# Kernel tuning notes

Measured on AMD Instinct MI355X. Metric: run time of the kernel, lower is better.

Reference implementation:

```python
import jax, jax.numpy as jnp
import numpy as np

B, D, T = 8, 1024, 512
HID, NH, NL = 256, 4, 2
OUT = HID // NH  # 64 per-head dim
ALPHA = 0.2      # leaky relu slope
EPS = 1e-5       # layernorm eps


def setup_inputs() -> dict:
    key = jax.random.key(0)
    ks = jax.random.split(key, 10)
    X_obs = jax.random.normal(ks[0], (B, D, T), dtype=jnp.float32)
    mask = (jax.random.uniform(ks[1], (B, D, T)) < 0.8).astype(jnp.float32)
    W_in = jax.random.normal(ks[2], (2 * T, HID), dtype=jnp.float32) * (1.0 / np.sqrt(2 * T))
    b_in = jnp.zeros((HID,), dtype=jnp.float32)
    gat_W = jax.random.normal(ks[3], (NL, NH, HID, OUT), dtype=jnp.float32) * (1.0 / np.sqrt(HID))
    gat_a = jax.random.normal(ks[4], (NL, NH, 2 * OUT), dtype=jnp.float32) * 0.1
    ln_g = jnp.ones((NL, HID), dtype=jnp.float32)
    ln_b = jnp.zeros((NL, HID), dtype=jnp.float32)
    W_out = jax.random.normal(ks[5], (HID, T), dtype=jnp.float32) * (1.0 / np.sqrt(HID))
    b_out = jnp.zeros((T,), dtype=jnp.float32)
    return dict(X_obs=X_obs, mask=mask, W_in=W_in, b_in=b_in, gat_W=gat_W,
                gat_a=gat_a, ln_g=ln_g, ln_b=ln_b, W_out=W_out, b_out=b_out)


def _layer_norm(x, g, b):
    mu = jnp.mean(x, axis=-1, keepdims=True)
    var = jnp.mean((x - mu) ** 2, axis=-1, keepdims=True)
    return (x - mu) * jax.lax.rsqrt(var + EPS) * g + b


def _gat_forward(X_obs, mask, W_in, b_in, gat_W, gat_a, ln_g, ln_b, W_out, b_out):
    # mean-impute per (d, t) position across batch
    obs_sum = jnp.sum(X_obs * mask, axis=0, keepdims=True)
    obs_cnt = jnp.sum(mask, axis=0, keepdims=True)
    pos_mean = obs_sum / (obs_cnt + 1e-10)
    X_mean = X_obs * mask + (1.0 - mask) * pos_mean

    x = jnp.concatenate([X_mean, mask], axis=-1)       # (B, D, 2T)
    h = x @ W_in + b_in                                 # (B, N, HID)

    for l in range(NL):
        Wl = gat_W[l]                                   # (H, HID, OUT)
        a_left = gat_a[l, :, :OUT]                      # (H, OUT)
        a_right = gat_a[l, :, OUT:]                     # (H, OUT)
        hW = jnp.einsum('bnd,hde->bhne', h, Wl)         # (B, H, N, OUT)
        # e_ij = leakyrelu(a_left . h_i + a_right . h_j) -- avoids O(N^2 * 2d) concat
        s_l = jnp.einsum('bhne,he->bhn', hW, a_left)
        s_r = jnp.einsum('bhne,he->bhn', hW, a_right)
        e = jax.nn.leaky_relu(s_l[..., :, None] + s_r[..., None, :], ALPHA)  # (B,H,N,N)
        attn = jax.nn.softmax(e, axis=-1)
        head_out = jnp.einsum('bhnm,bhme->bhne', attn, hW)                   # (B,H,N,OUT)
        h_new = jnp.transpose(head_out, (0, 2, 1, 3)).reshape(h.shape[0], h.shape[1], HID)
        h = _layer_norm(h + h_new, ln_g[l], ln_b[l])

    return h @ W_out + b_out                            # (B, D, T)


def reference(X_obs, mask, W_in, b_in, gat_W, gat_a, ln_g, ln_b, W_out, b_out):
    return _gat_forward(X_obs, mask, W_in, b_in, gat_W, gat_a, ln_g, ln_b, W_out, b_out)
```

## Files before the change

kernel.cpp:

```cpp
#include <hip/hip_runtime.h>
#include <hip/hip_bf16.h>

constexpr int B_   = 8;
constexpr int D_   = 1024;
constexpr int T_   = 512;
constexpr int HID_ = 256;
constexpr int NH_  = 4;
constexpr int NL_  = 2;
constexpr float ALPHA_ = 0.2f;
constexpr float EPS_   = 1e-5f;
constexpr int OUT_ = 64;
constexpr int M_ = B_ * D_;
constexpr int DT_ = D_ * T_;
constexpr int KIN_ = 2 * T_;

typedef __attribute__((ext_vector_type(8))) short short8;
typedef __attribute__((ext_vector_type(4))) float floatx4;

__device__ __forceinline__ unsigned short f2bf(float f) {
    unsigned int u = __float_as_uint(f);
    unsigned int r = u + 0x7fffu + ((u >> 16) & 1u);
    return (unsigned short)(r >> 16);
}
__device__ __forceinline__ unsigned int kenc(float f) {
    unsigned int u = __float_as_uint(f);
    return (u & 0x80000000u) ? ~u : (u | 0x80000000u);
}
__device__ __forceinline__ float kdec(unsigned int k) {
    unsigned int u = (k & 0x80000000u) ? (k ^ 0x80000000u) : ~k;
    return __uint_as_float(u);
}

__global__ __launch_bounds__(256) void prep_k(const float* __restrict__ X,
                                              const float* __restrict__ Mk,
                                              const float* __restrict__ W_in,
                                              const float* __restrict__ gatW,
                                              const float* __restrict__ W_out,
                                              unsigned short* __restrict__ Ain,
                                              unsigned short* __restrict__ Wt_in,
                                              unsigned short* __restrict__ Wcat,
                                              unsigned short* __restrict__ WtO,
                                              unsigned int* __restrict__ rmaxkey) {
    int bx = blockIdx.x;
    if (bx < 512) {
        int idx4 = (bx * 256 + threadIdx.x) * 4;
        int t = idx4 & (T_ - 1);
        int d = idx4 >> 9;
        float4 x[B_], m[B_];
        float4 s = {0, 0, 0, 0}, c = {0, 0, 0, 0};
#pragma unroll
        for (int b = 0; b < B_; b++) {
            x[b] = *(const float4*)&X[(size_t)b * DT_ + idx4];
            m[b] = *(const float4*)&Mk[(size_t)b * DT_ + idx4];
            s.x += x[b].x * m[b].x; s.y += x[b].y * m[b].y;
            s.z += x[b].z * m[b].z; s.w += x[b].w * m[b].w;
            c.x += m[b].x; c.y += m[b].y; c.z += m[b].z; c.w += m[b].w;
        }
        float4 pm;
        pm.x = s.x / (c.x + 1e-10f); pm.y = s.y / (c.y + 1e-10f);
        pm.z = s.z / (c.z + 1e-10f); pm.w = s.w / (c.w + 1e-10f);
#pragma unroll
        for (int b = 0; b < B_; b++) {
            size_t row = (size_t)b * D_ + d;
            ushort4 xm, mk;
            xm.x = f2bf(x[b].x * m[b].x + (1.f - m[b].x) * pm.x);
            xm.y = f2bf(x[b].y * m[b].y + (1.f - m[b].y) * pm.y);
            xm.z = f2bf(x[b].z * m[b].z + (1.f - m[b].z) * pm.z);
            xm.w = f2bf(x[b].w * m[b].w + (1.f - m[b].w) * pm.w);
            mk.x = f2bf(m[b].x); mk.y = f2bf(m[b].y);
            mk.z = f2bf(m[b].z); mk.w = f2bf(m[b].w);
            *(ushort4*)&Ain[row * KIN_ + t]      = xm;
            *(ushort4*)&Ain[row * KIN_ + T_ + t] = mk;
        }
    } else {
        int idx = (bx - 512) * 256 + threadIdx.x;
        if (idx < 64) rmaxkey[idx] = 0u;
        if (idx < 262144) {
            int n = idx >> 10, k = idx & 1023;
            Wt_in[idx] = f2bf(W_in[(size_t)k * HID_ + n]);
        } else if (idx < 393216) {
            int j = idx - 262144;
            int l = j >> 16, n = (j >> 8) & 255, k = j & 255;
            int h = n >> 6, e = n & 63;
            Wcat[j] = f2bf(gatW[(((size_t)(l * NH_ + h) * HID_) + k) * OUT_ + e]);
        } else {
            int j = idx - 393216;
            int n = j >> 8, k = j & 255;
            WtO[j] = f2bf(W_out[(size_t)k * T_ + n]);
        }
    }
}

template <int MODE>
__global__ __launch_bounds__(256) void gemm_bf16_k(
        const unsigned short* __restrict__ A,
        const unsigned short* __restrict__ Bt,
        const float* __restrict__ bias,
        float* __restrict__ C,
        unsigned short* __restrict__ Cb,
        const float* __restrict__ ga,
        float* __restrict__ s_l,
        float* __restrict__ s_r,
        unsigned int* __restrict__ rmaxkey,
        int Nsz, int Ksz) {
    __shared__ __align__(16) unsigned short As[2][64 * 72];
    __shared__ __align__(16) unsigned short Bs[2][64 * 72];
    int tid = threadIdx.x;
    int wave = tid >> 6, lane = tid & 63;
    int q = lane >> 4, r16 = lane & 15;
    int rowbase = blockIdx.y * 64;
    int colbase = blockIdx.x * 64;

    int srow = tid >> 3, sk = (tid & 7) * 8;
    const unsigned short* Ap0 = A + (size_t)(rowbase + srow) * Ksz + sk;
    const unsigned short* Ap1 = A + (size_t)(rowbase + srow + 32) * Ksz + sk;
    const unsigned short* Bp0 = Bt + (size_t)(colbase + srow) * Ksz + sk;
    const unsigned short* Bp1 = Bt + (size_t)(colbase + srow + 32) * Ksz + sk;
    int la0 = srow * 72 + sk, la1 = (srow + 32) * 72 + sk;

    floatx4 acc[4];
#pragma unroll
    for (int i = 0; i < 4; i++) acc[i] = (floatx4)0.f;

    uint4 pa0 = *(const uint4*)Ap0, pa1 = *(const uint4*)Ap1;
    uint4 pb0 = *(const uint4*)Bp0, pb1 = *(const uint4*)Bp1;
    *(uint4*)&As[0][la0] = pa0;
    *(uint4*)&As[0][la1] = pa1;
    *(uint4*)&Bs[0][la0] = pb0;
    *(uint4*)&Bs[0][la1] = pb1;

    int nk = Ksz >> 6;
    for (int it = 0; it < nk; it++) {
        int cur = it & 1;
        __syncthreads();
        if (it + 1 < nk) {
            int kt = (it + 1) << 6;
            pa0 = *(const uint4*)(Ap0 + kt);
            pa1 = *(const uint4*)(Ap1 + kt);
            pb0 = *(const uint4*)(Bp0 + kt);
            pb1 = *(const uint4*)(Bp1 + kt);
        }
#pragma unroll
        for (int t = 0; t < 2; t++) {
            short8 a = *(const short8*)&As[cur][(wave * 16 + r16) * 72 + t * 32 + q * 8];
#pragma unroll
            for (int ni = 0; ni < 4; ni++) {
                short8 b = *(const short8*)&Bs[cur][(ni * 16 + r16) * 72 + t * 32 + q * 8];
                acc[ni] = __builtin_amdgcn_mfma_f32_16x16x32_bf16(a, b, acc[ni], 0, 0, 0);
            }
        }
        if (it + 1 < nk) {
            int nxt = cur ^ 1;
            *(uint4*)&As[nxt][la0] = pa0;
            *(uint4*)&As[nxt][la1] = pa1;
            *(uint4*)&Bs[nxt][la0] = pb0;
            *(uint4*)&Bs[nxt][la1] = pb1;
        }
    }
    if constexpr (MODE == 2) {
        int bhh = ((rowbase >> 10) << 2) + blockIdx.x;
        int nb = (rowbase & (D_ - 1)) + wave * 16;
#pragma unroll
        for (int ni = 0; ni < 4; ni++) {
            int e = ni * 16 + r16;
            ushort4 pk;
            pk.x = f2bf(acc[ni][0]);
            pk.y = f2bf(acc[ni][1]);
            pk.z = f2bf(acc[ni][2]);
            pk.w = f2bf(acc[ni][3]);
            *(ushort4*)&Cb[((size_t)(bhh * 64 + e) << 10) + nb + q * 4] = pk;
        }
        const float* gab = ga + blockIdx.x * 2 * OUT_;
        float al4[4], ar4[4];
#pragma unroll
        for (int ni = 0; ni < 4; ni++) {
            al4[ni] = gab[ni * 16 + r16];
            ar4[ni] = gab[OUT_ + ni * 16 + r16];
        }
        float slv[4], srv[4];
#pragma unroll
        for (int rr = 0; rr < 4; rr++) {
            float s1 = 0.f, s2 = 0.f;
#pragma unroll
            for (int ni = 0; ni < 4; ni++) {
                s1 += acc[ni][rr] * al4[ni];
                s2 += acc[ni][rr] * ar4[ni];
            }
            slv[rr] = s1;
            srv[rr] = s2;
        }
#pragma unroll
        for (int off = 1; off < 16; off <<= 1) {
#pragma unroll
            for (int rr = 0; rr < 4; rr++) {
                slv[rr] += __shfl_xor(slv[rr], off, 64);
                srv[rr] += __shfl_xor(srv[rr], off, 64);
            }
        }
        {
            int rsel = r16 & 3;
            float sv = (rsel == 0) ? slv[0] : (rsel == 1) ? slv[1] : (rsel == 2) ? slv[2] : slv[3];
            float rv = (rsel == 0) ? srv[0] : (rsel == 1) ? srv[1] : (rsel == 2) ? srv[2] : srv[3];
            int n = nb + q * 4 + rsel;
            if (r16 < 4)                 s_l[bhh * D_ + n] = sv;
            else if (r16 >= 8 && r16 < 12) s_r[bhh * D_ + n] = rv;
        }
        float mx = fmaxf(fmaxf(srv[0], srv[1]), fmaxf(srv[2], srv[3]));
        mx = fmaxf(mx, __shfl_xor(mx, 16, 64));
        mx = fmaxf(mx, __shfl_xor(mx, 32, 64));
        if (lane == 0) atomicMax(&rmaxkey[bhh], kenc(mx));
    } else {
#pragma unroll
        for (int rr = 0; rr < 4; rr++) {
            int row = rowbase + wave * 16 + q * 4 + rr;
#pragma unroll
            for (int ni = 0; ni < 4; ni++) {
                int col = colbase + ni * 16 + r16;
                float v = acc[ni][rr] + (bias ? bias[col] : 0.f);
                C[(size_t)row * Nsz + col] = v;
                if constexpr (MODE == 1) Cb[(size_t)row * Nsz + col] = f2bf(v);
            }
        }
    }
}

__global__ __launch_bounds__(256) void attn_k(const unsigned short* __restrict__ hwT,
                                              const float* __restrict__ sl_g,
                                              const float* __restrict__ sr_g,
                                              const unsigned int* __restrict__ rmaxkey,
                                              float* __restrict__ pacc,
                                              float* __restrict__ pden) {
    int bh = blockIdx.x;
    int b = bh >> 2, h = bh & 3;
    int half = blockIdx.z;
    int mb = half * 512;
    int tid = threadIdx.x;
    int wave = tid >> 6, lane = tid & 63;
    int q = lane >> 4, r16 = lane & 15;

    __shared__ float srs[512];
    __shared__ __align__(16) unsigned short Vt[2][64][136];

    *(float2*)&srs[tid * 2] = *(const float2*)&sr_g[bh * D_ + mb + tid * 2];

    float rm = kdec(rmaxkey[bh]);
    int row0 = blockIdx.y * 64 + wave * 16;
    float sl = sl_g[bh * D_ + row0 + r16];
    float xm = sl + rm;
    float Mn = fmaxf(xm, ALPHA_ * xm);

    floatx4 acc[4];
#pragma unroll
    for (int i = 0; i < 4; i++) acc[i] = (floatx4)0.f;
    float dsum = 0.f;

    const unsigned short* vbase = hwT + ((size_t)(bh * 64) << 10) + mb;
    int se[4], sp[4];
#pragma unroll
    for (int i = 0; i < 4; i++) {
        int s = tid + i * 256;
        se[i] = s >> 4;
        sp[i] = (s & 15) * 8;
    }

    uint4 pre[4];
#pragma unroll
    for (int i = 0; i < 4; i++)
        pre[i] = *(const uint4*)&vbase[((size_t)se[i] << 10) + sp[i]];
#pragma unroll
    for (int i = 0; i < 4; i++)
        *(uint4*)&Vt[0][se[i]][sp[i]] = pre[i];
    __syncthreads();

    for (int c = 0; c < 4; c++) {
        int cur = c & 1;
        if (c < 3) {
            int mo = (c + 1) * 128;
#pragma unroll
            for (int i = 0; i < 4; i++)
                pre[i] = *(const uint4*)&vbase[((size_t)se[i] << 10) + mo + sp[i]];
        }
#pragma unroll
        for (int kk = 0; kk < 128; kk += 32) {
            int m0 = c * 128 + kk + q * 8;
            float4 s0 = *(const float4*)&srs[m0];
            float4 s1 = *(const float4*)&srs[m0 + 4];
            float sr8[8] = {s0.x, s0.y, s0.z, s0.w, s1.x, s1.y, s1.z, s1.w};
            float p[8];
#pragma unroll
            for (int j = 0; j < 8; j++) {
                float x = sl + sr8[j];
                float e = fmaxf(x, ALPHA_ * x);
                float pj = __expf(e - Mn);
                dsum += pj;
                p[j] = pj;
            }
            union { unsigned int u[4]; short8 s8; } cv;
#pragma unroll
            for (int j = 0; j < 4; j++) {
                unsigned int lo = (__float_as_uint(p[2 * j]) + 0x8000u) >> 16;
                unsigned int hi = (__float_as_uint(p[2 * j + 1]) + 0x8000u) & 0xffff0000u;
                cv.u[j] = hi | lo;
            }
#pragma unroll
            for (int ni = 0; ni < 4; ni++) {
                short8 bfr = *(const short8*)&Vt[cur][ni * 16 + r16][kk + q * 8];
                acc[ni] = __builtin_amdgcn_mfma_f32_16x16x32_bf16(cv.s8, bfr, acc[ni], 0, 0, 0);
            }
        }
        if (c < 3) {
#pragma unroll
            for (int i = 0; i < 4; i++)
                *(uint4*)&Vt[cur ^ 1][se[i]][sp[i]] = pre[i];
        }
        __syncthreads();
    }
    dsum += __shfl_xor(dsum, 16);
    dsum += __shfl_xor(dsum, 32);
    size_t gr0 = (size_t)b * D_ + row0;
    if (lane < 16) pden[((size_t)half * M_ + gr0 + r16) * NH_ + h] = dsum;
#pragma unroll
    for (int rr = 0; rr < 4; rr++) {
        size_t grow = gr0 + q * 4 + rr;
#pragma unroll
        for (int ni = 0; ni < 4; ni++) {
            pacc[((size_t)half * M_ + grow) * HID_ + h * OUT_ + ni * 16 + r16] = acc[ni][rr];
        }
    }
}

__global__ __launch_bounds__(256) void addln_k(float* __restrict__ h,
                                               const float* __restrict__ pacc,
                                               const float* __restrict__ pden,
                                               const float* __restrict__ g,
                                               const float* __restrict__ bb,
                                               unsigned short* __restrict__ hbf) {
    int wave = threadIdx.x >> 6, lane = threadIdx.x & 63;
    size_t row = (size_t)blockIdx.x * 4 + wave;
    float4 a  = *(const float4*)&h[row * HID_ + lane * 4];
    float4 p0 = *(const float4*)&pacc[row * HID_ + lane * 4];
    float4 p1 = *(const float4*)&pacc[((size_t)M_ + row) * HID_ + lane * 4];
    int hh = lane >> 4;
    float den = pden[row * NH_ + hh] + pden[((size_t)M_ + row) * NH_ + hh];
    float inv = 1.f / den;
    float4 v = {a.x + (p0.x + p1.x) * inv, a.y + (p0.y + p1.y) * inv,
                a.z + (p0.z + p1.z) * inv, a.w + (p0.w + p1.w) * inv};
    float s = v.x + v.y + v.z + v.w;
#pragma unroll
    for (int off = 1; off < 64; off <<= 1) s += __shfl_xor(s, off, 64);
    float mu = s * (1.f / HID_);
    float4 d = {v.x - mu, v.y - mu, v.z - mu, v.w - mu};
    float s2 = d.x * d.x + d.y * d.y + d.z * d.z + d.w * d.w;
#pragma unroll
    for (int off = 1; off < 64; off <<= 1) s2 += __shfl_xor(s2, off, 64);
    float rs = rsqrtf(s2 * (1.f / HID_) + EPS_);
    float4 gg = *(const float4*)&g[lane * 4];
    float4 bbv = *(const float4*)&bb[lane * 4];
    float4 res;
    res.x = d.x * rs * gg.x + bbv.x;
    res.y = d.y * rs * gg.y + bbv.y;
    res.z = d.z * rs * gg.z + bbv.z;
    res.w = d.w * rs * gg.w + bbv.w;
    *(float4*)&h[row * HID_ + lane * 4] = res;
    ushort4 pk = {f2bf(res.x), f2bf(res.y), f2bf(res.z), f2bf(res.w)};
    *(ushort4*)&hbf[row * HID_ + lane * 4] = pk;
}

extern "C" void kernel_launch(void* const* d_in, const int* in_sizes, int n_in,
                              void* d_out, int out_size, void* d_ws, size_t ws_size,
                              hipStream_t stream) {
    const float* X_obs = (const float*)d_in[0];
    const float* mask  = (const float*)d_in[1];
    const float* W_in  = (const float*)d_in[2];
    const float* b_in  = (const float*)d_in[3];
    const float* gat_W = (const float*)d_in[4];
    const float* gat_a = (const float*)d_in[5];
    const float* ln_g  = (const float*)d_in[6];
    const float* ln_b  = (const float*)d_in[7];
    const float* W_out = (const float*)d_in[8];
    const float* b_out = (const float*)d_in[9];
    float* out = (float*)d_out;

    char* base = (char*)d_ws;
    unsigned short* Ain  = (unsigned short*)base;
    unsigned short* hwT  = (unsigned short*)base;
    float* pacc = (float*)(base + (4u << 20));
    float* pden = (float*)(base + (20u << 20));
    float* hbuf = (float*)(base + (21u << 20));
    unsigned short* hbf   = (unsigned short*)(base + (29u << 20));
    unsigned short* Wt_in = (unsigned short*)(base + (33u << 20));
    unsigned short* Wcat  = Wt_in + (size_t)HID_ * KIN_;
    unsigned short* WtO   = Wcat + (size_t)NL_ * HID_ * HID_;
    float* slb = (float*)(WtO + (size_t)T_ * HID_);
    float* srb = slb + B_ * NH_ * D_;
    unsigned int* rmaxkey = (unsigned int*)(srb + B_ * NH_ * D_);

    prep_k<<<2560, 256, 0, stream>>>(X_obs, mask, W_in, gat_W, W_out,
                                     Ain, Wt_in, Wcat, WtO, rmaxkey);

    gemm_bf16_k<1><<<dim3(HID_ / 64, M_ / 64), 256, 0, stream>>>(
        Ain, Wt_in, b_in, hbuf, hbf, nullptr, nullptr, nullptr, nullptr,
        HID_, KIN_);

    for (int l = 0; l < NL_; l++) {
        gemm_bf16_k<2><<<dim3(HID_ / 64, M_ / 64), 256, 0, stream>>>(
            hbf, Wcat + (size_t)l * HID_ * HID_, nullptr, nullptr, hwT,
            gat_a + (size_t)l * NH_ * 2 * OUT_, slb, srb, rmaxkey + l * 32,
            HID_, HID_);
        attn_k<<<dim3(B_ * NH_, D_ / 64, 2), 256, 0, stream>>>(
            hwT, slb, srb, rmaxkey + l * 32, pacc, pden);
        addln_k<<<M_ / 4, 256, 0, stream>>>(hbuf, pacc, pden,
                                            ln_g + (size_t)l * HID_,
                                            ln_b + (size_t)l * HID_, hbf);
    }

    gemm_bf16_k<0><<<dim3(T_ / 64, M_ / 64), 256, 0, stream>>>(
        hbf, WtO, b_out, out, nullptr, nullptr, nullptr, nullptr, nullptr,
        T_, HID_);
}
```

Before: 217.0 us.

## Replace dense GAT attention with sorted prefix-sum decomposition of leaky-relu softmax

Uses the rank-1 structure of the attention logits (s_l[i] + s_r[j] through a piecewise-linear leaky relu). Each (batch, head) sorts s_r and builds prefix sums of exp-weighted values for both slopes. Each row then binary-searches its breakpoint and combines the two prefix sums, turning O(N^2) attention into O(N log N). This removes the dense MFMA attention kernel and fuses the residual add and layernorm into the row kernel. In exchange it adds a single-block-per-head bitonic sort and serial prefix scans with low parallelism, and it changes numerical behaviour by subtracting large prefix sums.

```diff
diff --git a/kernel.cpp b/kernel.cpp
--- a/kernel.cpp
+++ b/kernel.cpp
@@ -13,6 +13,7 @@
 constexpr int M_ = B_ * D_;
 constexpr int DT_ = D_ * T_;
 constexpr int KIN_ = 2 * T_;
+constexpr int CKS_ = 132;
 
 typedef __attribute__((ext_vector_type(8))) short short8;
 typedef __attribute__((ext_vector_type(4))) float floatx4;
@@ -21,6 +22,9 @@
     unsigned int u = __float_as_uint(f);
     unsigned int r = u + 0x7fffu + ((u >> 16) & 1u);
     return (unsigned short)(r >> 16);
+}
+__device__ __forceinline__ float bf2f(unsigned short u) {
+    return __uint_as_float(((unsigned int)u) << 16);
 }
 __device__ __forceinline__ unsigned int kenc(float f) {
     unsigned int u = __float_as_uint(f);
@@ -163,12 +167,11 @@
 #pragma unroll
         for (int ni = 0; ni < 4; ni++) {
             int e = ni * 16 + r16;
-            ushort4 pk;
-            pk.x = f2bf(acc[ni][0]);
-            pk.y = f2bf(acc[ni][1]);
-            pk.z = f2bf(acc[ni][2]);
-            pk.w = f2bf(acc[ni][3]);
-            *(ushort4*)&Cb[((size_t)(bhh * 64 + e) << 10) + nb + q * 4] = pk;
+#pragma unroll
+            for (int rr = 0; rr < 4; rr++) {
+                int m = nb + q * 4 + rr;
+                Cb[((size_t)bhh << 16) + ((size_t)m << 6) + e] = f2bf(acc[ni][rr]);
+            }
         }
         const float* gab = ga + blockIdx.x * 2 * OUT_;
         float al4[4], ar4[4];
@@ -224,146 +227,183 @@
     }
 }
 
-__global__ __launch_bounds__(256) void attn_k(const unsigned short* __restrict__ hwT,
-                                              const float* __restrict__ sl_g,
-                                              const float* __restrict__ sr_g,
-                                              const unsigned int* __restrict__ rmaxkey,
-                                              float* __restrict__ pacc,
-                                              float* __restrict__ pden) {
-    int bh = blockIdx.x;
-    int b = bh >> 2, h = bh & 3;
-    int half = blockIdx.z;
-    int mb = half * 512;
+__global__ __launch_bounds__(512) void sortprefix_k(
+        const unsigned short* __restrict__ hwN,
+        const float* __restrict__ sr_g,
+        const unsigned int* __restrict__ rmaxkey,
+        float* __restrict__ srt,
+        int* __restrict__ sig,
+        float* __restrict__ wm,
+        float* __restrict__ ck) {
+    __shared__ float skey[1024];
+    __shared__ int   sidx[1024];
+    __shared__ float w1s[1024], w2s[1024];
+    __shared__ float csum[8][64][2];
+    __shared__ float csca[8][2];
+    int bh = blockIdx.x, tid = threadIdx.x;
+    for (int t = tid; t < 1024; t += 512) { skey[t] = sr_g[bh * D_ + t]; sidx[t] = t; }
+    __syncthreads();
+    for (int k = 2; k <= 1024; k <<= 1) {
+        for (int j = k >> 1; j > 0; j >>= 1) {
+            for (int t = tid; t < 1024; t += 512) {
+                int ixj = t ^ j;
+                if (ixj > t) {
+                    bool up = ((t & k) == 0);
+                    float a = skey[t], b = skey[ixj];
+                    bool sw = up ? (a > b) : (a < b);
+                    if (sw) {
+                        skey[t] = b; skey[ixj] = a;
+                        int ti = sidx[t]; sidx[t] = sidx[ixj]; sidx[ixj] = ti;
+                    }
+                }
+            }
+            __syncthreads();
+        }
+    }
+    float rm = kdec(rmaxkey[bh]);
+    for (int t = tid; t < 1024; t += 512) {
+        float u = skey[t] - rm;
+        float w1 = __expf(u), w2 = __expf(ALPHA_ * u);
+        w1s[t] = w1; w2s[t] = w2;
+        srt[bh * D_ + t] = skey[t];
+        sig[bh * D_ + t] = sidx[t];
+        *(float2*)&wm[(size_t)(bh * D_ + t) * 2] = float2{w1, w2};
+    }
+    __syncthreads();
+    int e = tid & 63, c = tid >> 6;
+    const unsigned short* vb = hwN + ((size_t)bh << 16);
+    int t0 = c * 128;
+    float a1 = 0.f, a2 = 0.f, q1 = 0.f, q2 = 0.f;
+    for (int t = t0; t < t0 + 128; ++t) {
+        float v = bf2f(vb[((size_t)sidx[t] << 6) + e]);
+        a1 = fmaf(w1s[t], v, a1);
+        a2 = fmaf(w2s[t], v, a2);
+    }
+    csum[c][e][0] = a1; csum[c][e][1] = a2;
+    if (e == 0) {
+        for (int t = t0; t < t0 + 128; ++t) { q1 += w1s[t]; q2 += w2s[t]; }
+        csca[c][0] = q1; csca[c][1] = q2;
+    }
+    __syncthreads();
+    float r1 = 0.f, r2 = 0.f, p1 = 0.f, p2 = 0.f;
+    for (int cc = 0; cc < c; ++cc) { r1 += csum[cc][e][0]; r2 += csum[cc][e][1]; }
+    if (e == 0) {
+        for (int cc = 0; cc < c; ++cc) { p1 += csca[cc][0]; p2 += csca[cc][1]; }
+    }
+    float* ckb = ck + (size_t)bh * 257 * CKS_;
+    for (int t = t0; t < t0 + 128; ++t) {
+        if ((t & 3) == 0) {
+            *(float2*)&ckb[(size_t)(t >> 2) * CKS_ + 2 * e] = float2{r1, r2};
+            if (e == 0) *(float2*)&ckb[(size_t)(t >> 2) * CKS_ + 128] = float2{p1, p2};
+        }
+        float v = bf2f(vb[((size_t)sidx[t] << 6) + e]);
+        r1 = fmaf(w1s[t], v, r1);
+        r2 = fmaf(w2s[t], v, r2);
+        if (e == 0) { p1 += w1s[t]; p2 += w2s[t]; }
+    }
+    if (c == 7) {
+        *(float2*)&ckb[(size_t)256 * CKS_ + 2 * e] = float2{r1, r2};
+        if (e == 0) *(float2*)&ckb[(size_t)256 * CKS_ + 128] = float2{p1, p2};
+    }
+}
+
+__global__ __launch_bounds__(128) void rowln_k(
+        float* __restrict__ h,
+        const float* __restrict__ sl_g,
+        const unsigned int* __restrict__ rmaxkey,
+        const float* __restrict__ srt,
+        const int* __restrict__ sig,
+        const float* __restrict__ wm,
+        const float* __restrict__ ck,
+        const unsigned short* __restrict__ hwN,
+        const float* __restrict__ g,
+        const float* __restrict__ bb,
+        unsigned short* __restrict__ hbf) {
+    __shared__ float srtL[4][1024];
+    __shared__ float hnew[32][260];
+    int blk = blockIdx.x;
+    int b = blk >> 5;
+    int d0 = (blk & 31) << 5;
     int tid = threadIdx.x;
-    int wave = tid >> 6, lane = tid & 63;
-    int q = lane >> 4, r16 = lane & 15;
-
-    __shared__ float srs[512];
-    __shared__ __align__(16) unsigned short Vt[2][64][136];
-
-    *(float2*)&srs[tid * 2] = *(const float2*)&sr_g[bh * D_ + mb + tid * 2];
-
+    for (int i = tid; i < 4096; i += 128)
+        srtL[i >> 10][i & 1023] = srt[(size_t)((b * 4 + (i >> 10)) * D_) + (i & 1023)];
+    __syncthreads();
+    int r = tid & 31, h4 = tid >> 5;
+    int bh = b * 4 + h4;
+    int d = d0 + r;
+    float sl = sl_g[bh * D_ + d];
     float rm = kdec(rmaxkey[bh]);
-    int row0 = blockIdx.y * 64 + wave * 16;
-    float sl = sl_g[bh * D_ + row0 + r16];
-    float xm = sl + rm;
-    float Mn = fmaxf(xm, ALPHA_ * xm);
-
-    floatx4 acc[4];
-#pragma unroll
-    for (int i = 0; i < 4; i++) acc[i] = (floatx4)0.f;
-    float dsum = 0.f;
-
-    const unsigned short* vbase = hwT + ((size_t)(bh * 64) << 10) + mb;
-    int se[4], sp[4];
-#pragma unroll
-    for (int i = 0; i < 4; i++) {
-        int s = tid + i * 256;
-        se[i] = s >> 4;
-        sp[i] = (s & 15) * 8;
-    }
-
-    uint4 pre[4];
-#pragma unroll
-    for (int i = 0; i < 4; i++)
-        pre[i] = *(const uint4*)&vbase[((size_t)se[i] << 10) + sp[i]];
-#pragma unroll
-    for (int i = 0; i < 4; i++)
-        *(uint4*)&Vt[0][se[i]][sp[i]] = pre[i];
+    float x = sl + rm;
+    float Mn = fmaxf(x, ALPHA_ * x);
+    float A  = __expf(x - Mn);
+    float B2 = __expf(ALPHA_ * x - Mn);
+    float key = -sl;
+    int lo = 0, hi = 1024;
+    while (lo < hi) {
+        int mid = (lo + hi) >> 1;
+        if (srtL[h4][mid] < key) lo = mid + 1; else hi = mid;
+    }
+    int t = lo;
+    int c4 = t >> 2, nf = t & 3;
+    const float* ckb = ck + ((size_t)bh * 257 + c4) * CKS_;
+    const float* ckT = ck + ((size_t)bh * 257 + 256) * CKS_;
+    float2 qs = *(const float2*)&ckb[128];
+    float2 qT = *(const float2*)&ckT[128];
+    float w1f[3], w2f[3];
+    const unsigned short* vp[3];
+#pragma unroll
+    for (int f = 0; f < 3; ++f) {
+        w1f[f] = 0.f; w2f[f] = 0.f; vp[f] = hwN;
+        if (f < nf) {
+            int rk = c4 * 4 + f;
+            float2 ww = *(const float2*)&wm[(size_t)(bh * D_ + rk) * 2];
+            w1f[f] = ww.x; w2f[f] = ww.y;
+            vp[f] = hwN + ((size_t)bh << 16) + ((size_t)sig[bh * D_ + rk] << 6);
+            qs.x += ww.x; qs.y += ww.y;
+        }
+    }
+    float den = A * (qT.x - qs.x) + B2 * qs.y;
+    float inv = 1.f / den;
+    for (int e = 0; e < 64; ++e) {
+        float2 p  = *(const float2*)&ckb[2 * e];
+        float2 Tt = *(const float2*)&ckT[2 * e];
+#pragma unroll
+        for (int f = 0; f < 3; ++f) {
+            if (f < nf) {
+                float v = bf2f(vp[f][e]);
+                p.x = fmaf(w1f[f], v, p.x);
+                p.y = fmaf(w2f[f], v, p.y);
+            }
+        }
+        hnew[r][h4 * 64 + e] = (A * (Tt.x - p.x) + B2 * p.y) * inv;
+    }
     __syncthreads();
-
-    for (int c = 0; c < 4; c++) {
-        int cur = c & 1;
-        if (c < 3) {
-            int mo = (c + 1) * 128;
-#pragma unroll
-            for (int i = 0; i < 4; i++)
-                pre[i] = *(const uint4*)&vbase[((size_t)se[i] << 10) + mo + sp[i]];
-        }
-#pragma unroll
-        for (int kk = 0; kk < 128; kk += 32) {
-            int m0 = c * 128 + kk + q * 8;
-            float4 s0 = *(const float4*)&srs[m0];
-            float4 s1 = *(const float4*)&srs[m0 + 4];
-            float sr8[8] = {s0.x, s0.y, s0.z, s0.w, s1.x, s1.y, s1.z, s1.w};
-            float p[8];
-#pragma unroll
-            for (int j = 0; j < 8; j++) {
-                float x = sl + sr8[j];
-                float e = fmaxf(x, ALPHA_ * x);
-                float pj = __expf(e - Mn);
-                dsum += pj;
-                p[j] = pj;
-            }
-            union { unsigned int u[4]; short8 s8; } cv;
-#pragma unroll
-            for (int j = 0; j < 4; j++) {
-                unsigned int lo = (__float_as_uint(p[2 * j]) + 0x8000u) >> 16;
-                unsigned int hi = (__float_as_uint(p[2 * j + 1]) + 0x8000u) & 0xffff0000u;
-                cv.u[j] = hi | lo;
-            }
-#pragma unroll
-            for (int ni = 0; ni < 4; ni++) {
-                short8 bfr = *(const short8*)&Vt[cur][ni * 16 + r16][kk + q * 8];
-                acc[ni] = __builtin_amdgcn_mfma_f32_16x16x32_bf16(cv.s8, bfr, acc[ni], 0, 0, 0);
-            }
-        }
-        if (c < 3) {
-#pragma unroll
-            for (int i = 0; i < 4; i++)
-                *(uint4*)&Vt[cur ^ 1][se[i]][sp[i]] = pre[i];
-        }
-        __syncthreads();
-    }
-    dsum += __shfl_xor(dsum, 16);
-    dsum += __shfl_xor(dsum, 32);
-    size_t gr0 = (size_t)b * D_ + row0;
-    if (lane < 16) pden[((size_t)half * M_ + gr0 + r16) * NH_ + h] = dsum;
-#pragma unroll
-    for (int rr = 0; rr < 4; rr++) {
-        size_t grow = gr0 + q * 4 + rr;
-#pragma unroll
-        for (int ni = 0; ni < 4; ni++) {
-            pacc[((size_t)half * M_ + grow) * HID_ + h * OUT_ + ni * 16 + r16] = acc[ni][rr];
-        }
-    }
-}
-
-__global__ __launch_bounds__(256) void addln_k(float* __restrict__ h,
-                                               const float* __restrict__ pacc,
-                                               const float* __restrict__ pden,
-                                               const float* __restrict__ g,
-                                               const float* __restrict__ bb,
-                                               unsigned short* __restrict__ hbf) {
-    int wave = threadIdx.x >> 6, lane = threadIdx.x & 63;
-    size_t row = (size_t)blockIdx.x * 4 + wave;
-    float4 a  = *(const float4*)&h[row * HID_ + lane * 4];
-    float4 p0 = *(const float4*)&pacc[row * HID_ + lane * 4];
-    float4 p1 = *(const float4*)&pacc[((size_t)M_ + row) * HID_ + lane * 4];
-    int hh = lane >> 4;
-    float den = pden[row * NH_ + hh] + pden[((size_t)M_ + row) * NH_ + hh];
-    float inv = 1.f / den;
-    float4 v = {a.x + (p0.x + p1.x) * inv, a.y + (p0.y + p1.y) * inv,
-                a.z + (p0.z + p1.z) * inv, a.w + (p0.w + p1.w) * inv};
-    float s = v.x + v.y + v.z + v.w;
-#pragma unroll
-    for (int off = 1; off < 64; off <<= 1) s += __shfl_xor(s, off, 64);
-    float mu = s * (1.f / HID_);
-    float4 d = {v.x - mu, v.y - mu, v.z - mu, v.w - mu};
-    float s2 = d.x * d.x + d.y * d.y + d.z * d.z + d.w * d.w;
-#pragma unroll
-    for (int off = 1; off < 64; off <<= 1) s2 += __shfl_xor(s2, off, 64);
-    float rs = rsqrtf(s2 * (1.f / HID_) + EPS_);
-    float4 gg = *(const float4*)&g[lane * 4];
-    float4 bbv = *(const float4*)&bb[lane * 4];
-    float4 res;
-    res.x = d.x * rs * gg.x + bbv.x;
-    res.y = d.y * rs * gg.y + bbv.y;
-    res.z = d.z * rs * gg.z + bbv.z;
-    res.w = d.w * rs * gg.w + bbv.w;
-    *(float4*)&h[row * HID_ + lane * 4] = res;
-    ushort4 pk = {f2bf(res.x), f2bf(res.y), f2bf(res.z), f2bf(res.w)};
-    *(ushort4*)&hbf[row * HID_ + lane * 4] = pk;
+    int wv = tid >> 6, ln = tid & 63;
+    for (int rr = wv * 16; rr < wv * 16 + 16; ++rr) {
+        size_t grow = ((((size_t)b << 10) + d0 + rr) << 8);
+        float4 a  = *(const float4*)&h[grow + ln * 4];
+        float4 nv = *(const float4*)&hnew[rr][ln * 4];
+        float4 v = {a.x + nv.x, a.y + nv.y, a.z + nv.z, a.w + nv.w};
+        float s = v.x + v.y + v.z + v.w;
+#pragma unroll
+        for (int off = 1; off < 64; off <<= 1) s += __shfl_xor(s, off, 64);
+        float mu = s * (1.f / HID_);
+        float4 dd = {v.x - mu, v.y - mu, v.z - mu, v.w - mu};
+        float s2 = dd.x * dd.x + dd.y * dd.y + dd.z * dd.z + dd.w * dd.w;
+#pragma unroll
+        for (int off = 1; off < 64; off <<= 1) s2 += __shfl_xor(s2, off, 64);
+        float rs = rsqrtf(s2 * (1.f / HID_) + EPS_);
+        float4 gg = *(const float4*)&g[ln * 4];
+        float4 bv = *(const float4*)&bb[ln * 4];
+        float4 res;
+        res.x = dd.x * rs * gg.x + bv.x;
+        res.y = dd.y * rs * gg.y + bv.y;
+        res.z = dd.z * rs * gg.z + bv.z;
+        res.w = dd.w * rs * gg.w + bv.w;
+        *(float4*)&h[grow + ln * 4] = res;
+        ushort4 pk = {f2bf(res.x), f2bf(res.y), f2bf(res.z), f2bf(res.w)};
+        *(ushort4*)&hbf[grow + ln * 4] = pk;
+    }
 }
 
 extern "C" void kernel_launch(void* const* d_in, const int* in_sizes, int n_in,
@@ -382,10 +422,12 @@
     float* out = (float*)d_out;
 
     char* base = (char*)d_ws;
-    unsigned short* Ain  = (unsigned short*)base;
-    unsigned short* hwT  = (unsigned short*)base;
-    float* pacc = (float*)(base + (4u << 20));
-    float* pden = (float*)(base + (20u << 20));
+    unsigned short* Ain = (unsigned short*)base;
+    unsigned short* hwN = (unsigned short*)base;
+    float* ck   = (float*)(base + (5u << 20));
+    float* wm   = (float*)(base + (10u << 20));
+    float* srtb = (float*)(base + (11u << 20));
+    int*   sig  = (int*)(base + (12u << 20));
     float* hbuf = (float*)(base + (21u << 20));
     unsigned short* hbf   = (unsigned short*)(base + (29u << 20));
     unsigned short* Wt_in = (unsigned short*)(base + (33u << 20));
@@ -404,14 +446,15 @@
 
     for (int l = 0; l < NL_; l++) {
         gemm_bf16_k<2><<<dim3(HID_ / 64, M_ / 64), 256, 0, stream>>>(
-            hbf, Wcat + (size_t)l * HID_ * HID_, nullptr, nullptr, hwT,
+            hbf, Wcat + (size_t)l * HID_ * HID_, nullptr, nullptr, hwN,
             gat_a + (size_t)l * NH_ * 2 * OUT_, slb, srb, rmaxkey + l * 32,
             HID_, HID_);
-        attn_k<<<dim3(B_ * NH_, D_ / 64, 2), 256, 0, stream>>>(
-            hwT, slb, srb, rmaxkey + l * 32, pacc, pden);
-        addln_k<<<M_ / 4, 256, 0, stream>>>(hbuf, pacc, pden,
-                                            ln_g + (size_t)l * HID_,
-                                            ln_b + (size_t)l * HID_, hbf);
+        sortprefix_k<<<32, 512, 0, stream>>>(hwN, srb, rmaxkey + l * 32,
+                                             srtb, sig, wm, ck);
+        rowln_k<<<256, 128, 0, stream>>>(hbuf, slb, rmaxkey + l * 32,
+                                         srtb, sig, wm, ck, hwN,
+                                         ln_g + (size_t)l * HID_,
+                                         ln_b + (size_t)l * HID_, hbf);
     }
 
     gemm_bf16_k<0><<<dim3(T_ / 64, M_ / 64), 256, 0, stream>>>(
```

Measured after the change: 366.2 us. 1.69x slower.

## Replace dense GAT attention with sorted prefix-sum factorization of leaky-relu softmax

Applied to the files above, without the earlier changes.

Replaces the O(N^2) attention matmul with an exact factorization. Because leaky_relu(s_l+s_r) is piecewise linear, exp splits into exp(s_r) or exp(alpha*s_r) terms depending on the sign of s_l+s_r. The s_r values are bitonic-sorted per (batch, head), prefix sums of weighted V rows are built, and each row binary-searches its split point to combine two partial sums. The hW output is also transposed to node-major layout through shared memory to suit the gather. This trades tensor-core work for a serial scan in only 32 blocks of 1024 threads, which risks low occupancy and possible exp overflow or precision issues from the unnormalized weights.

```diff
diff --git a/kernel.cpp b/kernel.cpp
--- a/kernel.cpp
+++ b/kernel.cpp
@@ -21,6 +21,9 @@
     unsigned int u = __float_as_uint(f);
     unsigned int r = u + 0x7fffu + ((u >> 16) & 1u);
     return (unsigned short)(r >> 16);
+}
+__device__ __forceinline__ float bf2f(unsigned short u) {
+    return __uint_as_float(((unsigned int)u) << 16);
 }
 __device__ __forceinline__ unsigned int kenc(float f) {
     unsigned int u = __float_as_uint(f);
@@ -159,17 +162,8 @@
     }
     if constexpr (MODE == 2) {
         int bhh = ((rowbase >> 10) << 2) + blockIdx.x;
-        int nb = (rowbase & (D_ - 1)) + wave * 16;
-#pragma unroll
-        for (int ni = 0; ni < 4; ni++) {
-            int e = ni * 16 + r16;
-            ushort4 pk;
-            pk.x = f2bf(acc[ni][0]);
-            pk.y = f2bf(acc[ni][1]);
-            pk.z = f2bf(acc[ni][2]);
-            pk.w = f2bf(acc[ni][3]);
-            *(ushort4*)&Cb[((size_t)(bhh * 64 + e) << 10) + nb + q * 4] = pk;
-        }
+        int nb0 = rowbase & (D_ - 1);
+        int nb = nb0 + wave * 16;
         const float* gab = ga + blockIdx.x * 2 * OUT_;
         float al4[4], ar4[4];
 #pragma unroll
@@ -209,6 +203,21 @@
         mx = fmaxf(mx, __shfl_xor(mx, 16, 64));
         mx = fmaxf(mx, __shfl_xor(mx, 32, 64));
         if (lane == 0) atomicMax(&rmaxkey[bhh], kenc(mx));
+        __syncthreads();
+        unsigned short* st = &As[0][0];
+#pragma unroll
+        for (int ni = 0; ni < 4; ni++)
+#pragma unroll
+            for (int rr = 0; rr < 4; rr++)
+                st[(wave * 16 + q * 4 + rr) * 72 + ni * 16 + r16] = f2bf(acc[ni][rr]);
+        __syncthreads();
+#pragma unroll
+        for (int i = 0; i < 2; i++) {
+            int idx = tid * 2 + i;
+            int row = idx >> 3, seg = idx & 7;
+            uint4 v = *(const uint4*)&st[row * 72 + seg * 8];
+            *(uint4*)&Cb[((size_t)bhh << 16) + ((size_t)(nb0 + row) << 6) + seg * 8] = v;
+        }
     } else {
 #pragma unroll
         for (int rr = 0; rr < 4; rr++) {
@@ -224,127 +233,141 @@
     }
 }
 
-__global__ __launch_bounds__(256) void attn_k(const unsigned short* __restrict__ hwT,
-                                              const float* __restrict__ sl_g,
-                                              const float* __restrict__ sr_g,
-                                              const unsigned int* __restrict__ rmaxkey,
-                                              float* __restrict__ pacc,
-                                              float* __restrict__ pden) {
-    int bh = blockIdx.x;
-    int b = bh >> 2, h = bh & 3;
-    int half = blockIdx.z;
-    int mb = half * 512;
-    int tid = threadIdx.x;
-    int wave = tid >> 6, lane = tid & 63;
-    int q = lane >> 4, r16 = lane & 15;
-
-    __shared__ float srs[512];
-    __shared__ __align__(16) unsigned short Vt[2][64][136];
-
-    *(float2*)&srs[tid * 2] = *(const float2*)&sr_g[bh * D_ + mb + tid * 2];
-
+__global__ __launch_bounds__(1024) void attnfac_k(
+        const unsigned short* __restrict__ hwN,
+        const float* __restrict__ sl_g,
+        const float* __restrict__ sr_g,
+        const unsigned int* __restrict__ rmaxkey,
+        float* __restrict__ hnew) {
+    __shared__ float srtL[1024];
+    __shared__ unsigned short sidxL[1024];
+    __shared__ float ws1[1024], ws2[1024];
+    __shared__ float slL[1024];
+    __shared__ float ck1[129][64], ck2[129][64];
+    __shared__ float ckp[129][2];
+    __shared__ float csum1[16][64], csum2[16][64];
+    __shared__ float csca[16][2];
+
+    int bh = blockIdx.x, tid = threadIdx.x;
+    int wv = tid >> 6, e = tid & 63;
     float rm = kdec(rmaxkey[bh]);
-    int row0 = blockIdx.y * 64 + wave * 16;
-    float sl = sl_g[bh * D_ + row0 + r16];
-    float xm = sl + rm;
-    float Mn = fmaxf(xm, ALPHA_ * xm);
-
-    floatx4 acc[4];
-#pragma unroll
-    for (int i = 0; i < 4; i++) acc[i] = (floatx4)0.f;
-    float dsum = 0.f;
-
-    const unsigned short* vbase = hwT + ((size_t)(bh * 64) << 10) + mb;
-    int se[4], sp[4];
-#pragma unroll
-    for (int i = 0; i < 4; i++) {
-        int s = tid + i * 256;
-        se[i] = s >> 4;
-        sp[i] = (s & 15) * 8;
-    }
-
-    uint4 pre[4];
-#pragma unroll
-    for (int i = 0; i < 4; i++)
-        pre[i] = *(const uint4*)&vbase[((size_t)se[i] << 10) + sp[i]];
-#pragma unroll
-    for (int i = 0; i < 4; i++)
-        *(uint4*)&Vt[0][se[i]][sp[i]] = pre[i];
+
+    srtL[tid] = sr_g[bh * D_ + tid];
+    sidxL[tid] = (unsigned short)tid;
+    slL[tid] = sl_g[bh * D_ + tid];
     __syncthreads();
-
-    for (int c = 0; c < 4; c++) {
-        int cur = c & 1;
-        if (c < 3) {
-            int mo = (c + 1) * 128;
-#pragma unroll
-            for (int i = 0; i < 4; i++)
-                pre[i] = *(const uint4*)&vbase[((size_t)se[i] << 10) + mo + sp[i]];
-        }
-#pragma unroll
-        for (int kk = 0; kk < 128; kk += 32) {
-            int m0 = c * 128 + kk + q * 8;
-            float4 s0 = *(const float4*)&srs[m0];
-            float4 s1 = *(const float4*)&srs[m0 + 4];
-            float sr8[8] = {s0.x, s0.y, s0.z, s0.w, s1.x, s1.y, s1.z, s1.w};
-            float p[8];
-#pragma unroll
-            for (int j = 0; j < 8; j++) {
-                float x = sl + sr8[j];
-                float e = fmaxf(x, ALPHA_ * x);
-                float pj = __expf(e - Mn);
-                dsum += pj;
-                p[j] = pj;
-            }
-            union { unsigned int u[4]; short8 s8; } cv;
-#pragma unroll
-            for (int j = 0; j < 4; j++) {
-                unsigned int lo = (__float_as_uint(p[2 * j]) + 0x8000u) >> 16;
-                unsigned int hi = (__float_as_uint(p[2 * j + 1]) + 0x8000u) & 0xffff0000u;
-                cv.u[j] = hi | lo;
-            }
-#pragma unroll
-            for (int ni = 0; ni < 4; ni++) {
-                short8 bfr = *(const short8*)&Vt[cur][ni * 16 + r16][kk + q * 8];
-                acc[ni] = __builtin_amdgcn_mfma_f32_16x16x32_bf16(cv.s8, bfr, acc[ni], 0, 0, 0);
-            }
-        }
-        if (c < 3) {
-#pragma unroll
-            for (int i = 0; i < 4; i++)
-                *(uint4*)&Vt[cur ^ 1][se[i]][sp[i]] = pre[i];
-        }
-        __syncthreads();
-    }
-    dsum += __shfl_xor(dsum, 16);
-    dsum += __shfl_xor(dsum, 32);
-    size_t gr0 = (size_t)b * D_ + row0;
-    if (lane < 16) pden[((size_t)half * M_ + gr0 + r16) * NH_ + h] = dsum;
-#pragma unroll
-    for (int rr = 0; rr < 4; rr++) {
-        size_t grow = gr0 + q * 4 + rr;
-#pragma unroll
-        for (int ni = 0; ni < 4; ni++) {
-            pacc[((size_t)half * M_ + grow) * HID_ + h * OUT_ + ni * 16 + r16] = acc[ni][rr];
-        }
-    }
-}
-
-__global__ __launch_bounds__(256) void addln_k(float* __restrict__ h,
-                                               const float* __restrict__ pacc,
-                                               const float* __restrict__ pden,
-                                               const float* __restrict__ g,
-                                               const float* __restrict__ bb,
-                                               unsigned short* __restrict__ hbf) {
+    for (int k = 2; k <= 1024; k <<= 1) {
+        for (int j = k >> 1; j > 0; j >>= 1) {
+            int t = tid, ixj = t ^ j;
+            if (ixj > t) {
+                bool up = ((t & k) == 0);
+                float a = srtL[t], b2 = srtL[ixj];
+                bool sw = up ? (a > b2) : (a < b2);
+                if (sw) {
+                    srtL[t] = b2; srtL[ixj] = a;
+                    unsigned short ti = sidxL[t]; sidxL[t] = sidxL[ixj]; sidxL[ixj] = ti;
+                }
+            }
+            __syncthreads();
+        }
+    }
+    {
+        float u = srtL[tid] - rm;
+        ws1[tid] = __expf(u);
+        ws2[tid] = __expf(ALPHA_ * u);
+    }
+    __syncthreads();
+
+    const unsigned short* vb = hwN + ((size_t)bh << 16);
+    {
+        float a1 = 0.f, a2 = 0.f, q1 = 0.f, q2 = 0.f;
+        int t0 = wv * 64;
+        for (int j = 0; j < 64; ++j) {
+            int t = t0 + j;
+            if ((j & 7) == 0) {
+                int tc = wv * 8 + (j >> 3);
+                ck1[tc][e] = a1; ck2[tc][e] = a2;
+                if (e == 0) { ckp[tc][0] = q1; ckp[tc][1] = q2; }
+            }
+            float w1 = ws1[t], w2 = ws2[t];
+            float v = bf2f(vb[((size_t)sidxL[t] << 6) + e]);
+            a1 = fmaf(w1, v, a1);
+            a2 = fmaf(w2, v, a2);
+            q1 += w1; q2 += w2;
+        }
+        csum1[wv][e] = a1; csum2[wv][e] = a2;
+        if (e == 0) { csca[wv][0] = q1; csca[wv][1] = q2; }
+    }
+    __syncthreads();
+    {
+        float o1 = 0.f, o2 = 0.f, op1 = 0.f, op2 = 0.f;
+        for (int cc = 0; cc < wv; ++cc) {
+            o1 += csum1[cc][e]; o2 += csum2[cc][e];
+            op1 += csca[cc][0]; op2 += csca[cc][1];
+        }
+#pragma unroll
+        for (int j = 0; j < 8; ++j) {
+            ck1[wv * 8 + j][e] += o1;
+            ck2[wv * 8 + j][e] += o2;
+        }
+        if (e < 8) {
+            ckp[wv * 8 + e][0] += op1;
+            ckp[wv * 8 + e][1] += op2;
+        }
+        if (wv == 15) {
+            ck1[128][e] = o1 + csum1[15][e];
+            ck2[128][e] = o2 + csum2[15][e];
+            if (e == 0) {
+                ckp[128][0] = op1 + csca[15][0];
+                ckp[128][1] = op2 + csca[15][1];
+            }
+        }
+    }
+    __syncthreads();
+    int b = bh >> 2, h4 = bh & 3;
+    float qT1 = ckp[128][0];
+    float TOT1 = ck1[128][e];
+    for (int j = 0; j < 64; ++j) {
+        int n = wv * 64 + j;
+        float sl = slL[n];
+        float x = sl + rm;
+        float Mn = fmaxf(x, ALPHA_ * x);
+        float A  = __expf(x - Mn);
+        float B2 = __expf(ALPHA_ * x - Mn);
+        float key = -sl;
+        int lo = 0, hi = 1024;
+        while (lo < hi) {
+            int mid = (lo + hi) >> 1;
+            if (srtL[mid] < key) lo = mid + 1; else hi = mid;
+        }
+        int t = lo, c8 = t >> 3, nf = t & 7;
+        float P1 = ck1[c8][e], P2 = ck2[c8][e];
+        float qp1 = ckp[c8][0], qp2 = ckp[c8][1];
+        for (int f = 0; f < nf; ++f) {
+            int rk = (c8 << 3) + f;
+            float w1 = ws1[rk], w2 = ws2[rk];
+            float v = bf2f(vb[((size_t)sidxL[rk] << 6) + e]);
+            P1 = fmaf(w1, v, P1);
+            P2 = fmaf(w2, v, P2);
+            qp1 += w1; qp2 += w2;
+        }
+        float den = A * (qT1 - qp1) + B2 * qp2;
+        float inv = 1.f / den;
+        float outv = (A * (TOT1 - P1) + B2 * P2) * inv;
+        hnew[(((size_t)b << 10) + n) * HID_ + h4 * OUT_ + e] = outv;
+    }
+}
+
+__global__ __launch_bounds__(256) void addln2_k(float* __restrict__ h,
+                                                const float* __restrict__ hnew,
+                                                const float* __restrict__ g,
+                                                const float* __restrict__ bb,
+                                                unsigned short* __restrict__ hbf) {
     int wave = threadIdx.x >> 6, lane = threadIdx.x & 63;
     size_t row = (size_t)blockIdx.x * 4 + wave;
     float4 a  = *(const float4*)&h[row * HID_ + lane * 4];
-    float4 p0 = *(const float4*)&pacc[row * HID_ + lane * 4];
-    float4 p1 = *(const float4*)&pacc[((size_t)M_ + row) * HID_ + lane * 4];
-    int hh = lane >> 4;
-    float den = pden[row * NH_ + hh] + pden[((size_t)M_ + row) * NH_ + hh];
-    float inv = 1.f / den;
-    float4 v = {a.x + (p0.x + p1.x) * inv, a.y + (p0.y + p1.y) * inv,
-                a.z + (p0.z + p1.z) * inv, a.w + (p0.w + p1.w) * inv};
+    float4 nv = *(const float4*)&hnew[row * HID_ + lane * 4];
+    float4 v = {a.x + nv.x, a.y + nv.y, a.z + nv.z, a.w + nv.w};
     float s = v.x + v.y + v.z + v.w;
 #pragma unroll
     for (int off = 1; off < 64; off <<= 1) s += __shfl_xor(s, off, 64);
@@ -382,13 +405,12 @@
     float* out = (float*)d_out;
 
     char* base = (char*)d_ws;
-    unsigned short* Ain  = (unsigned short*)base;
-    unsigned short* hwT  = (unsigned short*)base;
-    float* pacc = (float*)(base + (4u << 20));
-    float* pden = (float*)(base + (20u << 20));
-    float* hbuf = (float*)(base + (21u << 20));
-    unsigned short* hbf   = (unsigned short*)(base + (29u << 20));
-    unsigned short* Wt_in = (unsigned short*)(base + (33u << 20));
+    unsigned short* Ain = (unsigned short*)base;
+    unsigned short* hwN = (unsigned short*)base;
+    float* hnew = (float*)(base + (4u << 20));
+    float* hbuf = (float*)(base + (23u << 20));
+    unsigned short* hbf   = (unsigned short*)(base + (31u << 20));
+    unsigned short* Wt_in = (unsigned short*)(base + (35u << 20));
     unsigned short* Wcat  = Wt_in + (size_t)HID_ * KIN_;
     unsigned short* WtO   = Wcat + (size_t)NL_ * HID_ * HID_;
     float* slb = (float*)(WtO + (size_t)T_ * HID_);
@@ -404,14 +426,14 @@
 
     for (int l = 0; l < NL_; l++) {
         gemm_bf16_k<2><<<dim3(HID_ / 64, M_ / 64), 256, 0, stream>>>(
-            hbf, Wcat + (size_t)l * HID_ * HID_, nullptr, nullptr, hwT,
+            hbf, Wcat + (size_t)l * HID_ * HID_, nullptr, nullptr, hwN,
             gat_a + (size_t)l * NH_ * 2 * OUT_, slb, srb, rmaxkey + l * 32,
             HID_, HID_);
-        attn_k<<<dim3(B_ * NH_, D_ / 64, 2), 256, 0, stream>>>(
-            hwT, slb, srb, rmaxkey + l * 32, pacc, pden);
-        addln_k<<<M_ / 4, 256, 0, stream>>>(hbuf, pacc, pden,
-                                            ln_g + (size_t)l * HID_,
-                                            ln_b + (size_t)l * HID_, hbf);
+        attnfac_k<<<32, 1024, 0, stream>>>(hwN, slb, srb, rmaxkey + l * 32,
+                                           hnew);
+        addln2_k<<<M_ / 4, 256, 0, stream>>>(hbuf, hnew,
+                                             ln_g + (size_t)l * HID_,
+                                             ln_b + (size_t)l * HID_, hbf);
     }
 
     gemm_bf16_k<0><<<dim3(T_ / 64, M_ / 64), 256, 0, stream>>>(
```

Measured after the change: 411.3 us. 1.9x slower.
